# Performance work log

Measured on AMD Instinct MI355X. Metric: run time of the kernel, lower is better.

## Reference

```python
import jax, jax.numpy as jnp
import numpy as np

NQ, NK, E, DIM, H = 100000, 100000, 1600000, 128, 8
DH = DIM // H
LN_EPS = 1e-5


def _prelu(x, w):
    return jnp.where(x >= 0, x, w * x)


def setup_inputs() -> dict:
    key = jax.random.key(0)
    ks = jax.random.split(key, 12)
    s = 1.0 / np.sqrt(DIM)
    return {
        "query": jax.random.normal(ks[0], (NQ, DIM), jnp.float32),
        "keys": jax.random.normal(ks[1], (NK, DIM), jnp.float32),
        "values": jax.random.normal(ks[2], (NK, DIM), jnp.float32),
        "query_idx": jax.random.randint(ks[3], (E,), 0, NQ),
        "key_idx": jax.random.randint(ks[4], (E,), 0, NK),
        "Wq": jax.random.normal(ks[5], (DIM, DIM), jnp.float32) * s,
        "bq": jnp.zeros((DIM,), jnp.float32),
        "Wk": jax.random.normal(ks[6], (DIM, DIM), jnp.float32) * s,
        "bk": jnp.zeros((DIM,), jnp.float32),
        "Wv": jax.random.normal(ks[7], (DIM, DIM), jnp.float32) * s,
        "bv": jnp.zeros((DIM,), jnp.float32),
        "Wp": jax.random.normal(ks[8], (DIM, DIM), jnp.float32) * s,
        "bp": jnp.zeros((DIM,), jnp.float32),
        "a": jax.random.normal(ks[9], (1, H, DH), jnp.float32) * 0.1,
        "prelu_w": jnp.full((1,), 0.25, jnp.float32),
        "ln_g": jnp.ones((DIM,), jnp.float32),
        "ln_b": jnp.zeros((DIM,), jnp.float32),
    }


def reference(query, keys, values, query_idx, key_idx, Wq, bq, Wk, bk, Wv, bv,
              Wp, bp, a, prelu_w, ln_g, ln_b):
    nq = query.shape[0]
    # node-level projections, then per-edge gather (project-then-gather branch)
    Qp = query @ Wq.T + bq                      # [NQ, DIM]
    Kp = keys @ Wk.T + bk                       # [NK, DIM]
    # per-edge additive attention score: [E, H, 1]
    e = (a * _prelu(Qp[query_idx] + Kp[key_idx], prelu_w).reshape(-1, H, DH)).sum(-1, keepdims=True)
    # segment max (index_reduce amax, initialized at global min, detached)
    min_attn = jnp.min(e)
    max_q = jnp.full((nq, H, 1), min_attn, e.dtype).at[query_idx].max(e)
    max_q = jax.lax.stop_gradient(max_q)
    # segment softmax
    exp_e = jnp.exp(e - max_q[query_idx])       # [E, H, 1]
    denom = jnp.zeros((nq, H, 1), e.dtype).at[query_idx].add(exp_e)
    denom = jnp.where(denom == 0, jnp.asarray(1.0, e.dtype), denom)
    # weighted value aggregation (value_idx == key_idx here)
    Vv = (values @ Wv.T + bv)[key_idx].reshape(-1, H, DH)  # [E, H, DH]
    msg = jnp.zeros((nq, H, DH), e.dtype).at[query_idx].add(exp_e * Vv)
    # output projection + residual + LayerNorm (dropout is identity at eval)
    x = query + ((msg / denom).reshape(nq, DIM) @ Wp.T + bp)
    mu = x.mean(-1, keepdims=True)
    var = ((x - mu) ** 2).mean(-1, keepdims=True)
    return (x - mu) / jnp.sqrt(var + LN_EPS) * ln_g + ln_b
```

## Files before the change

### kernel.cpp

```cpp
#include <hip/hip_runtime.h>
#include <hip/hip_bf16.h>

#define DIMN 128
#define LN_EPS 1e-5f
#define WPAD 136

typedef __bf16 bf16x8 __attribute__((ext_vector_type(8)));
typedef float f32x4 __attribute__((ext_vector_type(4)));

__device__ __forceinline__ float bf_even(uint32_t u) {
    union { uint32_t u; float f; } c; c.u = u << 16; return c.f;
}
__device__ __forceinline__ float bf_odd(uint32_t u) {
    union { uint32_t u; float f; } c; c.u = u & 0xffff0000u; return c.f;
}

__device__ __forceinline__ float head_reduce(float e) {
    int x = __float_as_int(e);
    e += __int_as_float(__builtin_amdgcn_ds_swizzle(x, 0x041F));
    x = __float_as_int(e);
    e += __int_as_float(__builtin_amdgcn_ds_swizzle(x, 0x081F));
    x = __float_as_int(e);
    e += __int_as_float(__builtin_amdgcn_ds_swizzle(x, 0x101F));
    return e;
}

__global__ __launch_bounds__(256) void k_prep(
        const float* __restrict__ Wq, const float* __restrict__ Wk,
        const float* __restrict__ Wv, const float* __restrict__ Wp,
        __bf16* __restrict__ wsplit, const int* __restrict__ qidx,
        int* __restrict__ counts, int* __restrict__ rank, int E) {
    int bi = blockIdx.x;
    if (bi < 256) {
        int w = bi >> 6;
        const float* W = (w == 0) ? Wq : (w == 1) ? Wk : (w == 2) ? Wv : Wp;
        __bf16* hi = wsplit + (size_t)w * 32768;
        __bf16* lo = hi + 16384;
        int i = (bi & 63) * 256 + threadIdx.x;
        float x = W[i];
        __bf16 h = (__bf16)x;
        hi[i] = h;
        lo[i] = (__bf16)(x - (float)h);
    } else {
        int i = (bi - 256) * 256 + threadIdx.x;
        if (i < E) rank[i] = atomicAdd(&counts[qidx[i]], 1);
    }
}

__global__ __launch_bounds__(256, 2) void k_proj3(
        const float* __restrict__ query, const float* __restrict__ keys,
        const float* __restrict__ values, const __bf16* __restrict__ wsplit,
        const float* __restrict__ bq, const float* __restrict__ bk,
        const float* __restrict__ bv, float* __restrict__ Qp,
        __bf16* __restrict__ KV, int NQ_, int NK_,
        const int* __restrict__ counts, int* __restrict__ offs,
        int* __restrict__ bsum, int nb, int chunk) {
    __shared__ int s[256];
    __shared__ __align__(16) __bf16 WH[128 * WPAD];
    __shared__ __align__(16) __bf16 WL[128 * WPAD];

    if ((int)blockIdx.x < nb) {
        int t = threadIdx.x;
        int i = blockIdx.x * 256 + t;
        int v = (i < NQ_) ? counts[i] : 0;
        s[t] = v;
        __syncthreads();
        for (int o = 1; o < 256; o <<= 1) {
            int x = (t >= o) ? s[t - o] : 0;
            __syncthreads();
            s[t] += x;
            __syncthreads();
        }
        if (i < NQ_) offs[i] = s[t] - v;
        if (t == 255) bsum[blockIdx.x] = s[t];
    }

    int lane = threadIdx.x & 63;
    int wid  = threadIdx.x >> 6;
    int r = lane & 15, g = lane >> 4;
    int rowoff = (wid >> 1) * 16;
    int chalf  = wid & 1;

    int ntq = (NQ_ + 31) >> 5;
    int ntk = (NK_ + 31) >> 5;
    int total = ntq + 2 * ntk;

    int t0 = blockIdx.x * chunk;
    int t1 = t0 + chunk; if (t1 > total) t1 = total;
    int staged = -1;
    float bias_n[4];

    for (int t = t0; t < t1; ++t) {
        int m, tt;
        if (t < ntq)            { m = 0; tt = t; }
        else if (t < ntq + ntk) { m = 1; tt = t - ntq; }
        else                    { m = 2; tt = t - ntq - ntk; }

        if (m != staged) {
            if (staged != -1) __syncthreads();
            const uint4* srcH = (const uint4*)(wsplit + (size_t)m * 32768);
            const uint4* srcL = (const uint4*)(wsplit + (size_t)m * 32768 + 16384);
#pragma unroll
            for (int it = 0; it < 8; ++it) {
                int cid = threadIdx.x + it * 256;
                int n = cid >> 4, c16 = cid & 15;
                *(uint4*)((char*)WH + n * (WPAD * 2) + c16 * 16) = srcH[cid];
                *(uint4*)((char*)WL + n * (WPAD * 2) + c16 * 16) = srcL[cid];
            }
            __syncthreads();
            staged = m;
            const float* bias = (m == 0) ? bq : (m == 1) ? bk : bv;
#pragma unroll
            for (int c = 0; c < 4; ++c) bias_n[c] = bias[(chalf * 4 + c) * 16 + r];
        }

        const float* X = (m == 0) ? query : (m == 1) ? keys : values;
        int M = (m == 0) ? NQ_ : NK_;
        int rb = tt * 32 + rowoff;
        int arow = rb + r; if (arow >= M) arow = M - 1;
        const float* xrow = X + (size_t)arow * DIMN;

        bf16x8 Ah[4], Al[4];
#pragma unroll
        for (int ks = 0; ks < 4; ++ks) {
            const float* px = xrow + ks * 32 + g * 8;
            f32x4 v0 = *(const f32x4*)(px);
            f32x4 v1 = *(const f32x4*)(px + 4);
#pragma unroll
            for (int i = 0; i < 4; ++i) {
                __bf16 h0 = (__bf16)v0[i];
                __bf16 h1 = (__bf16)v1[i];
                Ah[ks][i]     = h0;
                Ah[ks][i + 4] = h1;
                if (m == 0) {
                    Al[ks][i]     = (__bf16)(v0[i] - (float)h0);
                    Al[ks][i + 4] = (__bf16)(v1[i] - (float)h1);
                }
            }
        }

        f32x4 acc[4];
#pragma unroll
        for (int c = 0; c < 4; ++c) {
            acc[c] = (f32x4){0.f, 0.f, 0.f, 0.f};
            int n = (chalf * 4 + c) * 16 + r;
#pragma unroll
            for (int ks = 0; ks < 4; ++ks) {
                bf16x8 Bh = *(const bf16x8*)(WH + n * WPAD + ks * 32 + g * 8);
                acc[c] = __builtin_amdgcn_mfma_f32_16x16x32_bf16(Ah[ks], Bh, acc[c], 0, 0, 0);
                if (m == 0) {
                    bf16x8 Bl = *(const bf16x8*)(WL + n * WPAD + ks * 32 + g * 8);
                    acc[c] = __builtin_amdgcn_mfma_f32_16x16x32_bf16(Ah[ks], Bl, acc[c], 0, 0, 0);
                    acc[c] = __builtin_amdgcn_mfma_f32_16x16x32_bf16(Al[ks], Bh, acc[c], 0, 0, 0);
                }
            }
        }

        if (m == 0) {
#pragma unroll
            for (int c = 0; c < 4; ++c) {
                int n = (chalf * 4 + c) * 16 + r;
#pragma unroll
                for (int i = 0; i < 4; ++i) {
                    int row = rb + g * 4 + i;
                    if (row < M) Qp[(size_t)row * DIMN + n] = acc[c][i] + bias_n[c];
                }
            }
        } else {
            int vofs = (m == 2) ? 128 : 0;
#pragma unroll
            for (int c = 0; c < 4; ++c) {
                int n = (chalf * 4 + c) * 16 + r;
#pragma unroll
                for (int i = 0; i < 4; ++i) {
                    int row = rb + g * 4 + i;
                    if (row < M) KV[(size_t)row * 256 + vofs + n] = (__bf16)(acc[c][i] + bias_n[c]);
                }
            }
        }
    }
}

__global__ __launch_bounds__(1024) void k_scan2(int* __restrict__ bsum, int nb) {
    __shared__ int s[1024];
    int t = threadIdx.x;
    int v = (t < nb) ? bsum[t] : 0;
    s[t] = v;
    __syncthreads();
    for (int o = 1; o < 1024; o <<= 1) {
        int x = (t >= o) ? s[t - o] : 0;
        __syncthreads();
        s[t] += x;
        __syncthreads();
    }
    if (t < nb) bsum[t] = s[t];
}

__global__ void k_scatter(const int* __restrict__ qidx, const int* __restrict__ kidx,
                          const int* __restrict__ offs, const int* __restrict__ bsum,
                          const int* __restrict__ rank, int* __restrict__ skey, int E) {
    int i = blockIdx.x * 256 + threadIdx.x;
    if (i < E) {
        int q = qidx[i];
        int base = offs[q] + ((q >= 256) ? bsum[(q >> 8) - 1] : 0);
        skey[base + rank[i]] = kidx[i];
    }
}

__global__ __launch_bounds__(256) void k_attn(
        const float* __restrict__ Qp, const __bf16* __restrict__ KV,
        const int* __restrict__ offs, const int* __restrict__ bsum,
        const int* __restrict__ skey, const float* __restrict__ a,
        const float* __restrict__ prelu_w, float* __restrict__ msg,
        int NQ_, int E_) {
    int lane = threadIdx.x & 63;
    int q = blockIdx.x * 4 + (threadIdx.x >> 6);
    if (q >= NQ_) return;
    int d = lane * 2;
    float2 av = *(const float2*)(a + d);
    float a0 = av.x, a1 = av.y;
    float pw = prelu_w[0];
    float2 qv = *(const float2*)(Qp + (size_t)q * DIMN + d);
    float q0 = qv.x, q1 = qv.y;
    int beg = offs[q] + ((q >= 256) ? bsum[(q >> 8) - 1] : 0);
    int qn = q + 1;
    int end = (qn == NQ_) ? E_ : offs[qn] + ((qn >= 256) ? bsum[(qn >> 8) - 1] : 0);

    float den = 0.f, acc0 = 0.f, acc1 = 0.f;
    int j = beg;
    for (; j + 3 < end; j += 4) {
        int k0 = skey[j], k1 = skey[j + 1], k2 = skey[j + 2], k3 = skey[j + 3];
        const uint32_t* r0 = (const uint32_t*)(KV + ((size_t)k0 << 8));
        const uint32_t* r1 = (const uint32_t*)(KV + ((size_t)k1 << 8));
        const uint32_t* r2 = (const uint32_t*)(KV + ((size_t)k2 << 8));
        const uint32_t* r3 = (const uint32_t*)(KV + ((size_t)k3 << 8));
        uint32_t ku0 = r0[lane], ku1 = r1[lane], ku2 = r2[lane], ku3 = r3[lane];
        uint32_t vu0 = r0[64 + lane], vu1 = r1[64 + lane], vu2 = r2[64 + lane], vu3 = r3[64 + lane];

        float e0, e1, e2, e3;
        {
            float s0 = q0 + bf_even(ku0), s1 = q1 + bf_odd(ku0);
            s0 = s0 >= 0.f ? s0 : pw * s0;  s1 = s1 >= 0.f ? s1 : pw * s1;
            e0 = a0 * s0 + a1 * s1;
        }
        {
            float s0 = q0 + bf_even(ku1), s1 = q1 + bf_odd(ku1);
            s0 = s0 >= 0.f ? s0 : pw * s0;  s1 = s1 >= 0.f ? s1 : pw * s1;
            e1 = a0 * s0 + a1 * s1;
        }
        {
            float s0 = q0 + bf_even(ku2), s1 = q1 + bf_odd(ku2);
            s0 = s0 >= 0.f ? s0 : pw * s0;  s1 = s1 >= 0.f ? s1 : pw * s1;
            e2 = a0 * s0 + a1 * s1;
        }
        {
            float s0 = q0 + bf_even(ku3), s1 = q1 + bf_odd(ku3);
            s0 = s0 >= 0.f ? s0 : pw * s0;  s1 = s1 >= 0.f ? s1 : pw * s1;
            e3 = a0 * s0 + a1 * s1;
        }
        e0 = head_reduce(e0);
        e1 = head_reduce(e1);
        e2 = head_reduce(e2);
        e3 = head_reduce(e3);
        float w0 = __expf(e0), w1 = __expf(e1), w2 = __expf(e2), w3 = __expf(e3);
        den  += (w0 + w1) + (w2 + w3);
        acc0 += w0 * bf_even(vu0) + w1 * bf_even(vu1) + w2 * bf_even(vu2) + w3 * bf_even(vu3);
        acc1 += w0 * bf_odd(vu0)  + w1 * bf_odd(vu1)  + w2 * bf_odd(vu2)  + w3 * bf_odd(vu3);
    }
    for (; j < end; ++j) {
        int k = skey[j];
        const uint32_t* r_ = (const uint32_t*)(KV + ((size_t)k << 8));
        uint32_t ku = r_[lane], vu = r_[64 + lane];
        float s0 = q0 + bf_even(ku), s1 = q1 + bf_odd(ku);
        s0 = s0 >= 0.f ? s0 : pw * s0;  s1 = s1 >= 0.f ? s1 : pw * s1;
        float e = a0 * s0 + a1 * s1;
        e = head_reduce(e);
        float w = __expf(e);
        den += w;
        acc0 += w * bf_even(vu);
        acc1 += w * bf_odd(vu);
    }
    float inv = den > 0.f ? 1.f / den : 0.f;
    float2 o; o.x = acc0 * inv; o.y = acc1 * inv;
    *(float2*)(msg + (size_t)q * DIMN + d) = o;
}

__global__ __launch_bounds__(256, 2) void k_final(
        const float* __restrict__ msg, const __bf16* __restrict__ wh,
        const __bf16* __restrict__ wl, const float* __restrict__ bp,
        const float* __restrict__ query, const float* __restrict__ lng,
        const float* __restrict__ lnb, float* __restrict__ out, int M) {
    __shared__ __align__(16) __bf16 WH[128 * WPAD];
    __shared__ __align__(16) __bf16 WL[128 * WPAD];
    {
        const uint4* srcH = (const uint4*)wh;
        const uint4* srcL = (const uint4*)wl;
#pragma unroll
        for (int it = 0; it < 8; ++it) {
            int cid = threadIdx.x + it * 256;
            int n = cid >> 4, c16 = cid & 15;
            *(uint4*)((char*)WH + n * (WPAD * 2) + c16 * 16) = srcH[cid];
            *(uint4*)((char*)WL + n * (WPAD * 2) + c16 * 16) = srcL[cid];
        }
    }
    __syncthreads();

    int lane = threadIdx.x & 63;
    int wid  = threadIdx.x >> 6;
    int r = lane & 15, g = lane >> 4;
    int rb = blockIdx.x * 64 + wid * 16;

    int arow = rb + r; if (arow >= M) arow = M - 1;
    const float* xrow = msg + (size_t)arow * DIMN;
    bf16x8 Ah[4], Al[4];
#pragma unroll
    for (int ks = 0; ks < 4; ++ks) {
        const float* px = xrow + ks * 32 + g * 8;
        f32x4 v0 = *(const f32x4*)(px);
        f32x4 v1 = *(const f32x4*)(px + 4);
#pragma unroll
        for (int i = 0; i < 4; ++i) {
            __bf16 h0 = (__bf16)v0[i];
            __bf16 h1 = (__bf16)v1[i];
            Ah[ks][i]     = h0;
            Ah[ks][i + 4] = h1;
            Al[ks][i]     = (__bf16)(v0[i] - (float)h0);
            Al[ks][i + 4] = (__bf16)(v1[i] - (float)h1);
        }
    }
    float xv[8][4];
#pragma unroll
    for (int ct = 0; ct < 8; ++ct) {
        f32x4 acc = {0.f, 0.f, 0.f, 0.f};
        int n = ct * 16 + r;
#pragma unroll
        for (int ks = 0; ks < 4; ++ks) {
            bf16x8 Bh = *(const bf16x8*)(WH + n * WPAD + ks * 32 + g * 8);
            bf16x8 Bl = *(const bf16x8*)(WL + n * WPAD + ks * 32 + g * 8);
            acc = __builtin_amdgcn_mfma_f32_16x16x32_bf16(Ah[ks], Bh, acc, 0, 0, 0);
            acc = __builtin_amdgcn_mfma_f32_16x16x32_bf16(Ah[ks], Bl, acc, 0, 0, 0);
            acc = __builtin_amdgcn_mfma_f32_16x16x32_bf16(Al[ks], Bh, acc, 0, 0, 0);
        }
        float bn = bp[n];
#pragma unroll
        for (int i = 0; i < 4; ++i) {
            int row = rb + g * 4 + i;
            int rc = row < M ? row : M - 1;
            xv[ct][i] = acc[i] + bn + query[(size_t)rc * DIMN + n];
        }
    }
#pragma unroll
    for (int i = 0; i < 4; ++i) {
        float s = 0.f, ss = 0.f;
#pragma unroll
        for (int ct = 0; ct < 8; ++ct) { s += xv[ct][i]; ss += xv[ct][i] * xv[ct][i]; }
        s += __shfl_xor(s, 1, 64);  ss += __shfl_xor(ss, 1, 64);
        s += __shfl_xor(s, 2, 64);  ss += __shfl_xor(ss, 2, 64);
        s += __shfl_xor(s, 4, 64);  ss += __shfl_xor(ss, 4, 64);
        s += __shfl_xor(s, 8, 64);  ss += __shfl_xor(ss, 8, 64);
        float mean = s * (1.f / DIMN);
        float var  = ss * (1.f / DIMN) - mean * mean;
        float rstd = rsqrtf(var + LN_EPS);
        int row = rb + g * 4 + i;
#pragma unroll
        for (int ct = 0; ct < 8; ++ct) {
            int n = ct * 16 + r;
            if (row < M)
                out[(size_t)row * DIMN + n] = (xv[ct][i] - mean) * rstd * lng[n] + lnb[n];
        }
    }
}

extern "C" void kernel_launch(void* const* d_in, const int* in_sizes, int n_in,
                              void* d_out, int out_size, void* d_ws, size_t ws_size,
                              hipStream_t stream) {
    const float* query = (const float*)d_in[0];
    const float* keys  = (const float*)d_in[1];
    const float* values= (const float*)d_in[2];
    const int*   qidx  = (const int*)d_in[3];
    const int*   kidx  = (const int*)d_in[4];
    const float* Wq    = (const float*)d_in[5];
    const float* bq    = (const float*)d_in[6];
    const float* Wk    = (const float*)d_in[7];
    const float* bk    = (const float*)d_in[8];
    const float* Wv    = (const float*)d_in[9];
    const float* bv    = (const float*)d_in[10];
    const float* Wp    = (const float*)d_in[11];
    const float* bp    = (const float*)d_in[12];
    const float* a     = (const float*)d_in[13];
    const float* pw    = (const float*)d_in[14];
    const float* lng   = (const float*)d_in[15];
    const float* lnb   = (const float*)d_in[16];

    int NQ_ = in_sizes[0] / DIMN;
    int NK_ = in_sizes[1] / DIMN;
    int E_  = in_sizes[3];

    char* p = (char*)d_ws;
    __bf16* wsplit = (__bf16*)p;
    size_t off = (size_t)4 * 32768 * sizeof(__bf16);
    float*  Qp = (float*)(p + off);  off += (size_t)NQ_ * DIMN * 4;
    __bf16* KV = (__bf16*)(p + off); off += (size_t)NK_ * 256 * 2;
    int* counts = (int*)(p + off); off += (((size_t)NQ_ * 4) + 127) / 128 * 128;
    int* offs   = (int*)(p + off); off += (((size_t)NQ_ * 4) + 127) / 128 * 128;
    int* bsum   = (int*)(p + off); off += 1024 * 4;
    int* rank   = (int*)(p + off); off += (size_t)E_ * 4;
    int* skey   = (int*)(p + off); off += (size_t)E_ * 4;
    float* msg  = Qp;

    hipMemsetAsync(counts, 0, (size_t)NQ_ * 4, stream);

    int ge = (E_ + 255) / 256;
    int gm = (NQ_ + 63) / 64;
    int nb = (NQ_ + 255) / 256;

    k_prep<<<256 + ge, 256, 0, stream>>>(Wq, Wk, Wv, Wp, wsplit, qidx, counts, rank, E_);

    int ntq = (NQ_ + 31) >> 5;
    int ntk = (NK_ + 31) >> 5;
    int total = ntq + 2 * ntk;
    int chunk = 5;
    int gproj = (total + chunk - 1) / chunk;
    if (gproj < nb) gproj = nb;
    k_proj3<<<gproj, 256, 0, stream>>>(query, keys, values, wsplit, bq, bk, bv,
                                       Qp, KV, NQ_, NK_, counts, offs, bsum, nb, chunk);

    k_scan2<<<1, 1024, 0, stream>>>(bsum, nb);

    k_scatter<<<ge, 256, 0, stream>>>(qidx, kidx, offs, bsum, rank, skey, E_);

    k_attn<<<(NQ_ + 3) / 4, 256, 0, stream>>>(Qp, KV, offs, bsum, skey, a, pw, msg, NQ_, E_);

    k_final<<<gm, 256, 0, stream>>>(msg, wsplit + 3 * 32768, wsplit + 3 * 32768 + 16384,
                                    bp, query, lng, lnb, (float*)d_out, NQ_);
}
```

Measured before the change: 363.6 us.

## Split wavefront into four 16-lane groups processing separate edges with 16-byte loads

The attention kernel now has each 16-lane group of a wavefront handle a different edge, with each lane owning 8 contiguous dims read through uint4 loads, instead of the whole wave handling one edge with 2 dims per lane. Each head's score now needs only a single swizzle step (two lanes per head), and the four partial accumulators are combined across groups once at the end. The intent is fewer, wider gather loads, more edges in flight per wave and less per-edge cross-lane reduction. The cost is wasted lanes on ragged tails and extra cross-lane reductions at the end for every query, including those with few edges.

```diff
diff --git a/kernel.cpp b/kernel.cpp
--- a/kernel.cpp
+++ b/kernel.cpp
@@ -13,16 +13,6 @@
 }
 __device__ __forceinline__ float bf_odd(uint32_t u) {
     union { uint32_t u; float f; } c; c.u = u & 0xffff0000u; return c.f;
-}
-
-__device__ __forceinline__ float head_reduce(float e) {
-    int x = __float_as_int(e);
-    e += __int_as_float(__builtin_amdgcn_ds_swizzle(x, 0x041F));
-    x = __float_as_int(e);
-    e += __int_as_float(__builtin_amdgcn_ds_swizzle(x, 0x081F));
-    x = __float_as_int(e);
-    e += __int_as_float(__builtin_amdgcn_ds_swizzle(x, 0x101F));
-    return e;
 }
 
 __global__ __launch_bounds__(256) void k_prep(
@@ -207,6 +197,36 @@
     }
 }
 
+__device__ __forceinline__ float score8(uint4 ku, const f32x4& qa, const f32x4& qb,
+                                        const f32x4& aa, const f32x4& ab, float pw) {
+    float e, x;
+    x = qa[0] + bf_even(ku.x); x = x >= 0.f ? x : pw * x; e  = aa[0] * x;
+    x = qa[1] + bf_odd (ku.x); x = x >= 0.f ? x : pw * x; e += aa[1] * x;
+    x = qa[2] + bf_even(ku.y); x = x >= 0.f ? x : pw * x; e += aa[2] * x;
+    x = qa[3] + bf_odd (ku.y); x = x >= 0.f ? x : pw * x; e += aa[3] * x;
+    x = qb[0] + bf_even(ku.z); x = x >= 0.f ? x : pw * x; e += ab[0] * x;
+    x = qb[1] + bf_odd (ku.z); x = x >= 0.f ? x : pw * x; e += ab[1] * x;
+    x = qb[2] + bf_even(ku.w); x = x >= 0.f ? x : pw * x; e += ab[2] * x;
+    x = qb[3] + bf_odd (ku.w); x = x >= 0.f ? x : pw * x; e += ab[3] * x;
+    return e;
+}
+
+__device__ __forceinline__ void acc8(uint4 vu, float w, f32x4& c0, f32x4& c1) {
+    c0[0] += w * bf_even(vu.x); c0[1] += w * bf_odd(vu.x);
+    c0[2] += w * bf_even(vu.y); c0[3] += w * bf_odd(vu.y);
+    c1[0] += w * bf_even(vu.z); c1[1] += w * bf_odd(vu.z);
+    c1[2] += w * bf_even(vu.w); c1[3] += w * bf_odd(vu.w);
+}
+
+__device__ __forceinline__ float red1(float v) {
+    return v + __int_as_float(__builtin_amdgcn_ds_swizzle(__float_as_int(v), 0x041F));
+}
+__device__ __forceinline__ float redg(float v) {
+    v += __int_as_float(__builtin_amdgcn_ds_swizzle(__float_as_int(v), 0x401F));
+    v += __shfl_xor(v, 32, 64);
+    return v;
+}
+
 __global__ __launch_bounds__(256) void k_attn(
         const float* __restrict__ Qp, const __bf16* __restrict__ KV,
         const int* __restrict__ offs, const int* __restrict__ bsum,
@@ -216,73 +236,61 @@
     int lane = threadIdx.x & 63;
     int q = blockIdx.x * 4 + (threadIdx.x >> 6);
     if (q >= NQ_) return;
-    int d = lane * 2;
-    float2 av = *(const float2*)(a + d);
-    float a0 = av.x, a1 = av.y;
+    int l16 = lane & 15;
+    int grp = lane >> 4;
+    int d0 = l16 * 8;
+
+    f32x4 aa = *(const f32x4*)(a + d0);
+    f32x4 ab = *(const f32x4*)(a + d0 + 4);
+    f32x4 qa = *(const f32x4*)(Qp + (size_t)q * DIMN + d0);
+    f32x4 qb = *(const f32x4*)(Qp + (size_t)q * DIMN + d0 + 4);
     float pw = prelu_w[0];
-    float2 qv = *(const float2*)(Qp + (size_t)q * DIMN + d);
-    float q0 = qv.x, q1 = qv.y;
+
     int beg = offs[q] + ((q >= 256) ? bsum[(q >> 8) - 1] : 0);
     int qn = q + 1;
     int end = (qn == NQ_) ? E_ : offs[qn] + ((qn >= 256) ? bsum[(qn >> 8) - 1] : 0);
 
-    float den = 0.f, acc0 = 0.f, acc1 = 0.f;
+    float den = 0.f;
+    f32x4 c0 = {0.f, 0.f, 0.f, 0.f}, c1 = {0.f, 0.f, 0.f, 0.f};
     int j = beg;
-    for (; j + 3 < end; j += 4) {
-        int k0 = skey[j], k1 = skey[j + 1], k2 = skey[j + 2], k3 = skey[j + 3];
-        const uint32_t* r0 = (const uint32_t*)(KV + ((size_t)k0 << 8));
-        const uint32_t* r1 = (const uint32_t*)(KV + ((size_t)k1 << 8));
-        const uint32_t* r2 = (const uint32_t*)(KV + ((size_t)k2 << 8));
-        const uint32_t* r3 = (const uint32_t*)(KV + ((size_t)k3 << 8));
-        uint32_t ku0 = r0[lane], ku1 = r1[lane], ku2 = r2[lane], ku3 = r3[lane];
-        uint32_t vu0 = r0[64 + lane], vu1 = r1[64 + lane], vu2 = r2[64 + lane], vu3 = r3[64 + lane];
-
-        float e0, e1, e2, e3;
-        {
-            float s0 = q0 + bf_even(ku0), s1 = q1 + bf_odd(ku0);
-            s0 = s0 >= 0.f ? s0 : pw * s0;  s1 = s1 >= 0.f ? s1 : pw * s1;
-            e0 = a0 * s0 + a1 * s1;
-        }
-        {
-            float s0 = q0 + bf_even(ku1), s1 = q1 + bf_odd(ku1);
-            s0 = s0 >= 0.f ? s0 : pw * s0;  s1 = s1 >= 0.f ? s1 : pw * s1;
-            e1 = a0 * s0 + a1 * s1;
-        }
-        {
-            float s0 = q0 + bf_even(ku2), s1 = q1 + bf_odd(ku2);
-            s0 = s0 >= 0.f ? s0 : pw * s0;  s1 = s1 >= 0.f ? s1 : pw * s1;
-            e2 = a0 * s0 + a1 * s1;
-        }
-        {
-            float s0 = q0 + bf_even(ku3), s1 = q1 + bf_odd(ku3);
-            s0 = s0 >= 0.f ? s0 : pw * s0;  s1 = s1 >= 0.f ? s1 : pw * s1;
-            e3 = a0 * s0 + a1 * s1;
-        }
-        e0 = head_reduce(e0);
-        e1 = head_reduce(e1);
-        e2 = head_reduce(e2);
-        e3 = head_reduce(e3);
-        float w0 = __expf(e0), w1 = __expf(e1), w2 = __expf(e2), w3 = __expf(e3);
-        den  += (w0 + w1) + (w2 + w3);
-        acc0 += w0 * bf_even(vu0) + w1 * bf_even(vu1) + w2 * bf_even(vu2) + w3 * bf_even(vu3);
-        acc1 += w0 * bf_odd(vu0)  + w1 * bf_odd(vu1)  + w2 * bf_odd(vu2)  + w3 * bf_odd(vu3);
-    }
-    for (; j < end; ++j) {
-        int k = skey[j];
-        const uint32_t* r_ = (const uint32_t*)(KV + ((size_t)k << 8));
-        uint32_t ku = r_[lane], vu = r_[64 + lane];
-        float s0 = q0 + bf_even(ku), s1 = q1 + bf_odd(ku);
-        s0 = s0 >= 0.f ? s0 : pw * s0;  s1 = s1 >= 0.f ? s1 : pw * s1;
-        float e = a0 * s0 + a1 * s1;
-        e = head_reduce(e);
-        float w = __expf(e);
+    for (; j + 4 < end; j += 8) {
+        int kA = skey[j + grp];
+        int jB = j + 4 + grp;
+        int kB = skey[jB < end ? jB : end - 1];
+        const uint4* rA = (const uint4*)(KV + ((size_t)kA << 8));
+        const uint4* rB = (const uint4*)(KV + ((size_t)kB << 8));
+        uint4 kuA = rA[l16], vuA = rA[16 + l16];
+        uint4 kuB = rB[l16], vuB = rB[16 + l16];
+        float eA = red1(score8(kuA, qa, qb, aa, ab, pw));
+        float eB = red1(score8(kuB, qa, qb, aa, ab, pw));
+        float wA = __expf(eA);
+        float wB = (jB < end) ? __expf(eB) : 0.f;
+        den += wA + wB;
+        acc8(vuA, wA, c0, c1);
+        acc8(vuB, wB, c0, c1);
+    }
+    if (j < end) {
+        int jj = j + grp;
+        int k = skey[jj < end ? jj : end - 1];
+        const uint4* r_ = (const uint4*)(KV + ((size_t)k << 8));
+        uint4 ku = r_[l16], vu = r_[16 + l16];
+        float e = red1(score8(ku, qa, qb, aa, ab, pw));
+        float w = (jj < end) ? __expf(e) : 0.f;
         den += w;
-        acc0 += w * bf_even(vu);
-        acc1 += w * bf_odd(vu);
-    }
+        acc8(vu, w, c0, c1);
+    }
+
+#pragma unroll
+    for (int i = 0; i < 4; ++i) { c0[i] = redg(c0[i]); c1[i] = redg(c1[i]); }
+    den = redg(den);
     float inv = den > 0.f ? 1.f / den : 0.f;
-    float2 o; o.x = acc0 * inv; o.y = acc1 * inv;
-    *(float2*)(msg + (size_t)q * DIMN + d) = o;
+    if (grp == 0) {
+        f32x4 o0, o1;
+#pragma unroll
+        for (int i = 0; i < 4; ++i) { o0[i] = c0[i] * inv; o1[i] = c1[i] * inv; }
+        *(f32x4*)(msg + (size_t)q * DIMN + d0)     = o0;
+        *(f32x4*)(msg + (size_t)q * DIMN + d0 + 4) = o1;
+    }
 }
 
 __global__ __launch_bounds__(256, 2) void k_final(
```

New measurement: 361.9 us. About the same (-0.5%).
